# Kernel optimization log

Hardware: AMD Instinct MI355X
Metric: run time of the kernel (lower is better)

The kernel has to match this reference:

```python
import jax, jax.numpy as jnp
import numpy as np

B, T, C = 1, 1024, 2048
N = 64          # head_size
H = C // N      # 32 heads
D_W = 96        # max(32, round(1.8*sqrt(C)/32)*32)
D_A = 96
D_V = 64        # max(32, round(1.3*sqrt(C)/32)*32)
EPS = 1e-12     # F.normalize eps


def setup_inputs() -> dict:
    key = jax.random.key(0)
    ks = jax.random.split(key, 24)
    g = lambda i, shape, s=0.02: jax.random.normal(ks[i], shape, jnp.float32) * s
    return {
        "x": jax.random.normal(ks[0], (B, T, C), jnp.float32),
        "v_first": jax.random.normal(ks[1], (B, T, C), jnp.float32),
        "attention_mask": jnp.ones((B, T), jnp.float32),
        "w0": g(2, (1, 1, C), 0.1) - 0.5,
        "w1": g(3, (C, D_W)),
        "w2": g(4, (D_W, C)),
        "a0": g(5, (1, 1, C), 0.1),
        "a1": g(6, (C, D_A)),
        "a2": g(7, (D_A, C)),
        "v0": g(8, (1, 1, C), 0.1) + 1.0,
        "v1": g(9, (C, D_V)),
        "v2": g(10, (D_V, C)),
        "k_k": jnp.full((1, 1, C), 0.85, jnp.float32),
        "k_a": jnp.ones((1, 1, C), jnp.float32),
        "r_k": g(11, (H, N), 0.1),
        "Wr": g(12, (C, C)),   # pre-transposed Linear weights: y = x @ W
        "Wk": g(13, (C, C)),
        "Wv": g(14, (C, C)),
        "Wo": g(15, (C, C)),
    }


def rwkv7_scan(r, w, k, v, a, b, mask):
    """RWKV-7 recurrence (RUN_CUDA_RWKV7g). All of r,w,k,v,a,b are (B,T,C); mask (B,T).
    Per head: S_t = S_{t-1}*diag(exp(-exp(w_t))) + (S_{t-1} a_t) b_t^T + v_t k_t^T,
    out_t = S_t r_t.  Masked timesteps leave the state untouched."""
    rh, kh, vh, ah, bh = (t.reshape(B, T, H, N) for t in (r, k, v, a, b))
    dec = jnp.exp(-jnp.exp(w.reshape(B, T, H, N)))
    m = mask[:, :, None, None]
    dec = dec * m + (1.0 - m)            # no decay on padded steps
    kh, vh, ah, bh = kh * m, vh * m, ah * m, bh * m
    seq = tuple(jnp.moveaxis(t, 1, 0) for t in (dec, rh, kh, vh, ah, bh))
    s0 = jnp.zeros((B, H, N, N), r.dtype)  # state[...,i,j]: i=value dim, j=key dim

    def step(state, inp):
        d, rr, kk, vv, aa, bb = inp      # each (B,H,N)
        sa = jnp.einsum('bhij,bhj->bhi', state, aa)
        state = (state * d[:, :, None, :]
                 + sa[..., None] * bb[:, :, None, :]
                 + vv[..., None] * kk[:, :, None, :])
        return state, jnp.einsum('bhij,bhj->bhi', state, rr)

    _, out = jax.lax.scan(step, s0, seq)
    return jnp.moveaxis(out, 0, 1).reshape(B, T, C)


def reference(x, v_first, attention_mask, w0, w1, w2, a0, a1, a2,
              v0, v1, v2, k_k, k_a, r_k, Wr, Wk, Wv, Wo):
    r = x @ Wr
    k = x @ Wk
    v = x @ Wv
    w = -jax.nn.softplus(-(w0 + jnp.tanh(x @ w1) @ w2)) - 0.6
    # layer_id != 0: mix with v_first
    v = v + (v_first - v) * jax.nn.sigmoid(v0 + (x @ v1) @ v2)
    a = jax.nn.sigmoid(a0 + (x @ a1) @ a2)
    kk = k * k_k
    kkh = kk.reshape(B, T, H, N)
    kkh = kkh / jnp.maximum(jnp.linalg.norm(kkh, axis=-1, keepdims=True), EPS)
    kk = kkh.reshape(B, T, C)
    k = k * (1.0 + (a - 1.0) * k_a)
    o = rwkv7_scan(r, w, k, v, -kk, kk * a, attention_mask)
    rh, kh, vh = (t.reshape(B, T, H, N) for t in (r, k, v))
    o = o + ((rh * kh * r_k).sum(-1, keepdims=True) * vh).reshape(B, T, C)
    return (o @ Wo, v_first)
```

## Files before the change

### kernel.cpp

```cpp
#include <hip/hip_runtime.h>
#include <math.h>

#define T_LEN 1024
#define C_DIM 2048
#define H_N   32
#define HEAD  64
#define BTC   (T_LEN * C_DIM)
#define REC2  768
#define RKV_N 6144
#define NPAIR (T_LEN / 2)

typedef __attribute__((ext_vector_type(8))) __bf16 bf16x8;
typedef __attribute__((ext_vector_type(4))) float  f32x4;

__device__ __forceinline__ void gll16(const void* g, void* l) {
    __builtin_amdgcn_global_load_lds((const __attribute__((address_space(1))) void*)g,
                                     (__attribute__((address_space(3))) void*)l, 16, 0, 0);
}

__device__ __forceinline__ float hex_add(float x) {
    int a = __builtin_amdgcn_mov_dpp(__float_as_int(x), 0xB1, 0xF, 0xF, true);
    float y = x + __int_as_float(a);
    int b = __builtin_amdgcn_mov_dpp(__float_as_int(y), 0x4E, 0xF, 0xF, true);
    float z = y + __int_as_float(b);
    int c = __builtin_amdgcn_mov_dpp(__float_as_int(z), 0x141, 0xF, 0xF, true);
    float w = z + __int_as_float(c);
    int d = __builtin_amdgcn_mov_dpp(__float_as_int(w), 0x140, 0xF, 0xF, true);
    return w + __int_as_float(d);
}

__global__ void cast_bf16_k(const float* __restrict__ s, __bf16* __restrict__ d, int n) {
    int i = blockIdx.x * 256 + threadIdx.x;
    if (i < n) d[i] = (__bf16)s[i];
}
__global__ void tanh_cast_k(const float* __restrict__ s, __bf16* __restrict__ d, int n) {
    int i = blockIdx.x * 256 + threadIdx.x;
    if (i < n) d[i] = (__bf16)tanhf(s[i]);
}

__global__ void transpose_cast_k(const float* __restrict__ src, __bf16* __restrict__ dst,
                                 int R, int C) {
    __shared__ float tile[32][33];
    int c0 = blockIdx.x * 32, r0 = blockIdx.y * 32;
    int tx = threadIdx.x, ty = threadIdx.y;
#pragma unroll
    for (int i = 0; i < 32; i += 8)
        tile[ty + i][tx] = src[(size_t)(r0 + ty + i) * C + c0 + tx];
    __syncthreads();
#pragma unroll
    for (int i = 0; i < 32; i += 8)
        dst[(size_t)(c0 + ty + i) * R + r0 + tx] = (__bf16)tile[tx][ty + i];
}

__global__ __launch_bounds__(256) void gemm_lds_64x128(
    const __bf16* __restrict__ A, const __bf16* __restrict__ BT,
    float* __restrict__ O, int M, int N, int K) {
    __shared__ __bf16 As[64 * 32];
    __shared__ __bf16 Bs[128 * 32];
    int tid  = threadIdx.x;
    int lane = tid & 63;
    int wv   = tid >> 6;
    int m    = lane & 15;
    int q    = lane >> 4;
    int wr   = wv >> 1, wc = wv & 1;
    int row0 = blockIdx.x * 64;
    int col0 = blockIdx.y * 128;

    int srow  = tid >> 2;
    int skoff = (tid & 3) * 8;
    const __bf16* agp = A  + (size_t)(row0 + srow) * K + skoff;
    const __bf16* bgp = BT + (size_t)(col0 + srow) * K + skoff;
    __bf16* alp = As + (size_t)(tid & ~63) * 8;
    __bf16* blp = Bs + (size_t)(tid & ~63) * 8;

    f32x4 acc[2][4];
#pragma unroll
    for (int i = 0; i < 2; i++)
#pragma unroll
        for (int j = 0; j < 4; j++) acc[i][j] = {0.f, 0.f, 0.f, 0.f};

    for (int k0 = 0; k0 < K; k0 += 32) {
        gll16(agp + k0, alp);
        gll16(bgp + k0, blp);
        gll16(bgp + (size_t)64 * K + k0, blp + 64 * 32);
        __syncthreads();

        bf16x8 af[2], bfv[4];
#pragma unroll
        for (int i = 0; i < 2; i++)
            af[i] = *(const bf16x8*)&As[(wr * 32 + i * 16 + m) * 32 + q * 8];
#pragma unroll
        for (int j = 0; j < 4; j++)
            bfv[j] = *(const bf16x8*)&Bs[(wc * 64 + j * 16 + m) * 32 + q * 8];
#pragma unroll
        for (int i = 0; i < 2; i++)
#pragma unroll
            for (int j = 0; j < 4; j++)
                acc[i][j] = __builtin_amdgcn_mfma_f32_16x16x32_bf16(af[i], bfv[j], acc[i][j], 0, 0, 0);
        __syncthreads();
    }

#pragma unroll
    for (int i = 0; i < 2; i++) {
        int orow = row0 + wr * 32 + i * 16 + q * 4;
#pragma unroll
        for (int j = 0; j < 4; j++) {
            int ocol = col0 + wc * 64 + j * 16 + m;
#pragma unroll
            for (int t = 0; t < 4; t++)
                O[(size_t)(orow + t) * N + ocol] = acc[i][j][t];
        }
    }
}

__global__ __launch_bounds__(64) void gemm_bt_w16(
    const __bf16* __restrict__ A, const __bf16* __restrict__ BT,
    float* __restrict__ O, int M, int N, int K) {
    int lane = threadIdx.x & 63;
    int m = lane & 15, q = lane >> 4;
    int row0 = blockIdx.x * 16;
    int col0 = blockIdx.y * 16;
    const __bf16* ap = A  + (size_t)(row0 + m) * K + q * 8;
    const __bf16* bp = BT + (size_t)(col0 + m) * K + q * 8;
    f32x4 acc = {0.f,0.f,0.f,0.f};
    for (int k0 = 0; k0 < K; k0 += 32) {
        bf16x8 av = *(const bf16x8*)(ap + k0);
        bf16x8 bv = *(const bf16x8*)(bp + k0);
        acc = __builtin_amdgcn_mfma_f32_16x16x32_bf16(av, bv, acc, 0, 0, 0);
    }
    int orow = row0 + q * 4;
    int ocol = col0 + m;
#pragma unroll
    for (int i = 0; i < 4; i++)
        O[(size_t)(orow + i) * N + ocol] = acc[i];
}

__global__ __launch_bounds__(64) void prep2_k(
    float* __restrict__ rkv,
    const float* __restrict__ vfirst,
    const float* __restrict__ ywb, const float* __restrict__ yab,
    const float* __restrict__ yvb,
    float* __restrict__ pk,
    const float* __restrict__ w0, const float* __restrict__ a0,
    const float* __restrict__ v0, const float* __restrict__ k_k,
    const float* __restrict__ k_a, const float* __restrict__ amask) {
    int tp = blockIdx.x >> 5;
    int h  = blockIdx.x & 31;
    int n  = threadIdx.x;
    int cc = h * HEAD + n;

    float d[2], a[2], bv[2], k[2], v[2], r[2];
#pragma unroll
    for (int s = 0; s < 2; ++s) {
        int t = 2 * tp + s;
        int idx = t * C_DIM + cc;
        size_t idx6 = (size_t)t * RKV_N + cc;
        float m  = amask[t];
        float rr = rkv[idx6];
        float kv = rkv[idx6 + 2048];
        float vv = rkv[idx6 + 4096];
        float wv = w0[cc] + ywb[idx];
        float wfin = -log1pf(expf(-wv)) - 0.6f;
        float dec  = expf(-expf(wfin));
        float sv   = 1.f / (1.f + expf(-(v0[cc] + yvb[idx])));
        float vnew = fmaf(vfirst[idx] - vv, sv, vv);
        float av   = 1.f / (1.f + expf(-(a0[cc] + yab[idx])));
        float kkp  = kv * k_k[cc];
        float ss = kkp * kkp;
#pragma unroll
        for (int off = 32; off > 0; off >>= 1) ss += __shfl_xor(ss, off);
        float kkn  = kkp / fmaxf(sqrtf(ss), 1e-12f);
        float knew = kv * (1.f + (av - 1.f) * k_a[cc]);
        d[s]  = dec * m + (1.f - m);
        a[s]  = -kkn * m;
        bv[s] = kkn * av * m;
        k[s]  = knew * m;
        v[s]  = vnew * m;
        r[s]  = rr;
        rkv[idx6 + 2048] = knew;
        rkv[idx6 + 4096] = vnew;
    }

    float dba = bv[0] * a[1];
    float dka = k[0]  * a[1];
    float dbr = bv[0] * r[0];
    float dkr = k[0]  * r[0];
#pragma unroll
    for (int off = 32; off > 0; off >>= 1) {
        dba += __shfl_xor(dba, off);
        dka += __shfl_xor(dka, off);
        dbr += __shfl_xor(dbr, off);
        dkr += __shfl_xor(dkr, off);
    }

    size_t rec = ((size_t)tp * H_N + h) * REC2;
    pk[rec + n]        = a[0];
    pk[rec + 64 + n]   = d[0] * a[1];
    pk[rec + 128 + n]  = fmaf(dbr, a[0], d[0] * r[0]);
    pk[rec + 192 + n]  = d[0] * d[1];
    pk[rec + 256 + n]  = fmaf(dba, bv[1], d[1] * bv[0]);
    pk[rec + 320 + n]  = bv[1];
    pk[rec + 384 + n]  = fmaf(dka, bv[1], d[1] * k[0]);
    pk[rec + 448 + n]  = k[1];
    pk[rec + 512 + n]  = r[1];
    pk[rec + 576 + n]  = v[0];
    pk[rec + 640 + n]  = v[1];
    if (n == 0) pk[rec + 704] = dkr;
}

__global__ __launch_bounds__(64, 1) void scan_k(
    const float* __restrict__ pk, float* __restrict__ out) {
    int b = blockIdx.x;
    int xcd  = b & 7;
    int rest = b >> 3;
    int hi   = rest & 3;
    int g    = rest >> 2;
    int h    = xcd + 8 * hi;

    int lane = threadIdx.x;
    int r = lane >> 4;
    int c = lane & 15;
    int row = g * 4 + r;
    int jb  = c * 4;

    float S0 = 0.f, S1 = 0.f, S2 = 0.f, S3 = 0.f;

    float4 A1R[4], A2R[4], R1R[4], DDR[4], B1R[4], B2R[4], C1R[4], C2R[4], R2R[4];
    float  v1R[4], v2R[4], g1R[4];

    const size_t tstep = (size_t)H_N * REC2;
    const float* base = pk + (size_t)h * REC2;

#define LOADSLOT(S_, T_) do {                          \
    const float* L_ = base + (size_t)(T_) * tstep;     \
    A1R[S_] = *(const float4*)(L_ + jb);               \
    A2R[S_] = *(const float4*)(L_ + 64 + jb);          \
    R1R[S_] = *(const float4*)(L_ + 128 + jb);         \
    DDR[S_] = *(const float4*)(L_ + 192 + jb);         \
    B1R[S_] = *(const float4*)(L_ + 256 + jb);         \
    B2R[S_] = *(const float4*)(L_ + 320 + jb);         \
    C1R[S_] = *(const float4*)(L_ + 384 + jb);         \
    C2R[S_] = *(const float4*)(L_ + 448 + jb);         \
    R2R[S_] = *(const float4*)(L_ + 512 + jb);         \
    v1R[S_] = L_[576 + row];                           \
    v2R[S_] = L_[640 + row];                           \
    g1R[S_] = L_[704];                                 \
} while (0)

#pragma unroll
    for (int s = 0; s < 4; ++s) LOADSLOT(s, s);
    __builtin_amdgcn_sched_barrier(0);

    int off = h * HEAD;

#pragma unroll 1
    for (int tp0 = 0; tp0 < NPAIR; tp0 += 4) {
#pragma unroll
        for (int s = 0; s < 4; ++s) {
            int tp = tp0 + s;
            float4 A1v = A1R[s], A2v = A2R[s], R1v = R1R[s], DDv = DDR[s];
            float4 B1v = B1R[s], B2v = B2R[s], C1v = C1R[s], C2v = C2R[s];
            float4 R2v = R2R[s];
            float  vv1 = v1R[s], vv2 = v2R[s], gg1 = g1R[s];
            int tn = tp + 4;
            if (tn > NPAIR - 1) tn = NPAIR - 1;
            LOADSLOT(s, tn);
            __builtin_amdgcn_sched_barrier(0);

            float pa = fmaf(S0, A1v.x, S1 * A1v.y);
            float qa = fmaf(S2, A1v.z, S3 * A1v.w);
            float pb = fmaf(S0, A2v.x, S1 * A2v.y);
            float qb = fmaf(S2, A2v.z, S3 * A2v.w);
            float pr = fmaf(S0, R1v.x, S1 * R1v.y);
            float qr = fmaf(S2, R1v.z, S3 * R1v.w);
            float sa1 = hex_add(pa + qa);
            float sa2 = hex_add(pb + qb);
            float so1 = hex_add(pr + qr);
            if (c == 0) out[off + row] = fmaf(gg1, vv1, so1);

            float t0c = fmaf(vv1, C1v.x, vv2 * C2v.x);
            float t1c = fmaf(vv1, C1v.y, vv2 * C2v.y);
            float t2c = fmaf(vv1, C1v.z, vv2 * C2v.z);
            float t3c = fmaf(vv1, C1v.w, vv2 * C2v.w);
            float z0 = fmaf(sa1, B1v.x, t0c);
            float z1 = fmaf(sa1, B1v.y, t1c);
            float z2 = fmaf(sa1, B1v.z, t2c);
            float z3 = fmaf(sa1, B1v.w, t3c);
            float y0 = fmaf(sa2, B2v.x, z0);
            float y1 = fmaf(sa2, B2v.y, z1);
            float y2 = fmaf(sa2, B2v.z, z2);
            float y3 = fmaf(sa2, B2v.w, z3);
            S0 = fmaf(DDv.x, S0, y0);
            S1 = fmaf(DDv.y, S1, y1);
            S2 = fmaf(DDv.z, S2, y2);
            S3 = fmaf(DDv.w, S3, y3);

            float o0 = fmaf(S0, R2v.x, S1 * R2v.y);
            float o1 = fmaf(S2, R2v.z, S3 * R2v.w);
            float op = hex_add(o0 + o1);
            if (c == 0) out[off + C_DIM + row] = op;
            off += 2 * C_DIM;
            __builtin_amdgcn_sched_barrier(0);
        }
    }
#undef LOADSLOT
}

__global__ __launch_bounds__(64) void resid_k(
    const float* __restrict__ rkv, const float* __restrict__ souts,
    const float* __restrict__ r_k, const float* __restrict__ vfirst,
    __bf16* __restrict__ ob, float* __restrict__ dout) {
    int t = blockIdx.x >> 5;
    int h = blockIdx.x & 31;
    int n = threadIdx.x;
    int cc  = h * HEAD + n;
    int idx = t * C_DIM + cc;
    size_t idx6 = (size_t)t * RKV_N + cc;
    float s = rkv[idx6] * rkv[idx6 + 2048] * r_k[cc];
#pragma unroll
    for (int off = 32; off > 0; off >>= 1) s += __shfl_xor(s, off);
    float ov = souts[idx] + s * rkv[idx6 + 4096];
    ob[idx] = (__bf16)ov;
    dout[BTC + idx] = vfirst[idx];
}

extern "C" void kernel_launch(void* const* d_in, const int* in_sizes, int n_in,
                              void* d_out, int out_size, void* d_ws, size_t ws_size,
                              hipStream_t stream) {
    const float* x      = (const float*)d_in[0];
    const float* vfirst = (const float*)d_in[1];
    const float* amask  = (const float*)d_in[2];
    const float* w0 = (const float*)d_in[3];
    const float* w1 = (const float*)d_in[4];
    const float* w2 = (const float*)d_in[5];
    const float* a0 = (const float*)d_in[6];
    const float* a1 = (const float*)d_in[7];
    const float* a2 = (const float*)d_in[8];
    const float* v0 = (const float*)d_in[9];
    const float* v1 = (const float*)d_in[10];
    const float* v2 = (const float*)d_in[11];
    const float* k_k = (const float*)d_in[12];
    const float* k_a = (const float*)d_in[13];
    const float* r_k = (const float*)d_in[14];
    const float* Wr = (const float*)d_in[15];
    const float* Wk = (const float*)d_in[16];
    const float* Wv = (const float*)d_in[17];
    const float* Wo = (const float*)d_in[18];
    float* dout = (float*)d_out;

    char* wp = (char*)d_ws;
    auto alloc = [&](size_t bytes) -> void* {
        void* p = (void*)wp;
        wp += (bytes + 255) & ~(size_t)255;
        return p;
    };
    __bf16* xb   = (__bf16*)alloc((size_t)BTC * 2);
    __bf16* rkvT = (__bf16*)alloc((size_t)3 * C_DIM * C_DIM * 2);
    __bf16* WoT  = (__bf16*)alloc((size_t)C_DIM * C_DIM * 2);
    __bf16* w1T = (__bf16*)alloc((size_t)96 * C_DIM * 2);
    __bf16* a1T = (__bf16*)alloc((size_t)96 * C_DIM * 2);
    __bf16* v1T = (__bf16*)alloc((size_t)64 * C_DIM * 2);
    __bf16* w2T = (__bf16*)alloc((size_t)C_DIM * 96 * 2);
    __bf16* a2T = (__bf16*)alloc((size_t)C_DIM * 96 * 2);
    __bf16* v2T = (__bf16*)alloc((size_t)C_DIM * 64 * 2);
    float*  rkv = (float*)alloc((size_t)T_LEN * RKV_N * 4);
    float*  hw  = (float*)alloc((size_t)T_LEN * 96 * 4);
    float*  ha  = (float*)alloc((size_t)T_LEN * 96 * 4);
    float*  hv  = (float*)alloc((size_t)T_LEN * 64 * 4);
    __bf16* hwb = (__bf16*)alloc((size_t)T_LEN * 96 * 2);
    __bf16* hab = (__bf16*)alloc((size_t)T_LEN * 96 * 2);
    __bf16* hvb = (__bf16*)alloc((size_t)T_LEN * 64 * 2);
    float*  ywb = (float*)alloc((size_t)BTC * 4);
    float*  yab = (float*)alloc((size_t)BTC * 4);
    float*  yvb = (float*)alloc((size_t)BTC * 4);
    float*  pk  = (float*)alloc((size_t)NPAIR * H_N * REC2 * 4 + 4096);
    float*  souts = (float*)alloc((size_t)BTC * 4);
    __bf16* ob  = (__bf16*)alloc((size_t)BTC * 2);

    cast_bf16_k<<<dim3(BTC / 256), 256, 0, stream>>>(x, xb, BTC);

    dim3 tb(32, 8);
    transpose_cast_k<<<dim3(64, 64), tb, 0, stream>>>(Wr, rkvT, C_DIM, C_DIM);
    transpose_cast_k<<<dim3(64, 64), tb, 0, stream>>>(Wk, rkvT + (size_t)C_DIM * C_DIM, C_DIM, C_DIM);
    transpose_cast_k<<<dim3(64, 64), tb, 0, stream>>>(Wv, rkvT + (size_t)2 * C_DIM * C_DIM, C_DIM, C_DIM);
    transpose_cast_k<<<dim3(64, 64), tb, 0, stream>>>(Wo, WoT, C_DIM, C_DIM);
    transpose_cast_k<<<dim3(3, 64), tb, 0, stream>>>(w1, w1T, C_DIM, 96);
    transpose_cast_k<<<dim3(3, 64), tb, 0, stream>>>(a1, a1T, C_DIM, 96);
    transpose_cast_k<<<dim3(2, 64), tb, 0, stream>>>(v1, v1T, C_DIM, 64);
    transpose_cast_k<<<dim3(64, 3), tb, 0, stream>>>(w2, w2T, 96, C_DIM);
    transpose_cast_k<<<dim3(64, 3), tb, 0, stream>>>(a2, a2T, 96, C_DIM);
    transpose_cast_k<<<dim3(64, 2), tb, 0, stream>>>(v2, v2T, 64, C_DIM);

    gemm_lds_64x128<<<dim3(16, 48), 256, 0, stream>>>(xb, rkvT, rkv, T_LEN, RKV_N, C_DIM);

    gemm_bt_w16<<<dim3(64, 6), 64, 0, stream>>>(xb, w1T, hw, T_LEN, 96, C_DIM);
    gemm_bt_w16<<<dim3(64, 6), 64, 0, stream>>>(xb, a1T, ha, T_LEN, 96, C_DIM);
    gemm_bt_w16<<<dim3(64, 4), 64, 0, stream>>>(xb, v1T, hv, T_LEN, 64, C_DIM);

    tanh_cast_k<<<dim3((T_LEN * 96 + 255) / 256), 256, 0, stream>>>(hw, hwb, T_LEN * 96);
    cast_bf16_k<<<dim3((T_LEN * 96 + 255) / 256), 256, 0, stream>>>(ha, hab, T_LEN * 96);
    cast_bf16_k<<<dim3((T_LEN * 64 + 255) / 256), 256, 0, stream>>>(hv, hvb, T_LEN * 64);

    gemm_lds_64x128<<<dim3(16, 16), 256, 0, stream>>>(hwb, w2T, ywb, T_LEN, C_DIM, 96);
    gemm_lds_64x128<<<dim3(16, 16), 256, 0, stream>>>(hab, a2T, yab, T_LEN, C_DIM, 96);
    gemm_lds_64x128<<<dim3(16, 16), 256, 0, stream>>>(hvb, v2T, yvb, T_LEN, C_DIM, 64);

    prep2_k<<<dim3(NPAIR * H_N), 64, 0, stream>>>(rkv, vfirst, ywb, yab, yvb,
                                                  pk, w0, a0, v0, k_k, k_a, amask);

    scan_k<<<dim3(H_N * 16), 64, 0, stream>>>(pk, souts);

    resid_k<<<dim3(T_LEN * H_N), 64, 0, stream>>>(rkv, souts, r_k, vfirst, ob, dout);

    gemm_lds_64x128<<<dim3(16, 16), 256, 0, stream>>>(ob, WoT, dout, T_LEN, C_DIM, C_DIM);
}
```

Baseline: 528.1 us.

## Batch weight transposes and LoRA GEMMs into fewer launches, pack scan v/residual loads

Merges the ten transpose kernels into one z-indexed launch. The three first-stage LoRA GEMMs become one N=256 GEMM with a fused tanh/cast pass, and the three second-stage LoRA GEMMs become one z-batched launch. The scan record packs v1, v2 and the precomputed dkr*v into a single float4 per row, replacing three scalar loads and an fma. The aim is to cut launch count and scan load latency, at the cost of a larger pk record (REC2 768 to 832) and some early-exit blocks in the transpose grid.

New measurement: 475.4 us. 1.11x faster.

```diff
diff --git a/kernel.cpp b/kernel.cpp
--- a/kernel.cpp
+++ b/kernel.cpp
@@ -6,7 +6,7 @@
 #define H_N   32
 #define HEAD  64
 #define BTC   (T_LEN * C_DIM)
-#define REC2  768
+#define REC2  832
 #define RKV_N 6144
 #define NPAIR (T_LEN / 2)
 
@@ -33,15 +33,28 @@
     int i = blockIdx.x * 256 + threadIdx.x;
     if (i < n) d[i] = (__bf16)s[i];
 }
-__global__ void tanh_cast_k(const float* __restrict__ s, __bf16* __restrict__ d, int n) {
+
+__global__ void act_lora1_k(const float* __restrict__ s, __bf16* __restrict__ d) {
     int i = blockIdx.x * 256 + threadIdx.x;
-    if (i < n) d[i] = (__bf16)tanhf(s[i]);
-}
-
-__global__ void transpose_cast_k(const float* __restrict__ src, __bf16* __restrict__ dst,
-                                 int R, int C) {
+    float v = s[i];
+    if ((i & 255) < 96) v = tanhf(v);
+    d[i] = (__bf16)v;
+}
+
+struct TransBatch {
+    const float* s[10];
+    __bf16*      d[10];
+    int R[10];
+    int C[10];
+};
+__global__ void transpose_batch_k(TransBatch tb) {
+    int z = blockIdx.z;
+    const float* src = tb.s[z];
+    __bf16* dst = tb.d[z];
+    int R = tb.R[z], C = tb.C[z];
+    int c0 = blockIdx.x * 32, r0 = blockIdx.y * 32;
+    if (c0 >= C || r0 >= R) return;
     __shared__ float tile[32][33];
-    int c0 = blockIdx.x * 32, r0 = blockIdx.y * 32;
     int tx = threadIdx.x, ty = threadIdx.y;
 #pragma unroll
     for (int i = 0; i < 32; i += 8)
@@ -69,6 +82,78 @@
     int srow  = tid >> 2;
     int skoff = (tid & 3) * 8;
     const __bf16* agp = A  + (size_t)(row0 + srow) * K + skoff;
+    const __bf16* bgp = BT + (size_t)(col0 + srow) * K + skoff;
+    __bf16* alp = As + (size_t)(tid & ~63) * 8;
+    __bf16* blp = Bs + (size_t)(tid & ~63) * 8;
+
+    f32x4 acc[2][4];
+#pragma unroll
+    for (int i = 0; i < 2; i++)
+#pragma unroll
+        for (int j = 0; j < 4; j++) acc[i][j] = {0.f, 0.f, 0.f, 0.f};
+
+    for (int k0 = 0; k0 < K; k0 += 32) {
+        gll16(agp + k0, alp);
+        gll16(bgp + k0, blp);
+        gll16(bgp + (size_t)64 * K + k0, blp + 64 * 32);
+        __syncthreads();
+
+        bf16x8 af[2], bfv[4];
+#pragma unroll
+        for (int i = 0; i < 2; i++)
+            af[i] = *(const bf16x8*)&As[(wr * 32 + i * 16 + m) * 32 + q * 8];
+#pragma unroll
+        for (int j = 0; j < 4; j++)
+            bfv[j] = *(const bf16x8*)&Bs[(wc * 64 + j * 16 + m) * 32 + q * 8];
+#pragma unroll
+        for (int i = 0; i < 2; i++)
+#pragma unroll
+            for (int j = 0; j < 4; j++)
+                acc[i][j] = __builtin_amdgcn_mfma_f32_16x16x32_bf16(af[i], bfv[j], acc[i][j], 0, 0, 0);
+        __syncthreads();
+    }
+
+#pragma unroll
+    for (int i = 0; i < 2; i++) {
+        int orow = row0 + wr * 32 + i * 16 + q * 4;
+#pragma unroll
+        for (int j = 0; j < 4; j++) {
+            int ocol = col0 + wc * 64 + j * 16 + m;
+#pragma unroll
+            for (int t = 0; t < 4; t++)
+                O[(size_t)(orow + t) * N + ocol] = acc[i][j][t];
+        }
+    }
+}
+
+struct Lora2Cfg {
+    const __bf16* A[3];
+    const __bf16* BT[3];
+    float*        O[3];
+    int K[3];
+};
+__global__ __launch_bounds__(256) void gemm_lora2_k(Lora2Cfg cfg) {
+    const int LDA = 256, N = C_DIM;
+    int z = blockIdx.z;
+    const __bf16* A  = cfg.A[z];
+    const __bf16* BT = cfg.BT[z];
+    float* O = cfg.O[z];
+    int K = cfg.K[z];
+
+    __shared__ __bf16 As[64 * 32];
+    __shared__ __bf16 Bs[128 * 32];
+    int tid  = threadIdx.x;
+    int lane = tid & 63;
+    int wv   = tid >> 6;
+    int m    = lane & 15;
+    int q    = lane >> 4;
+    int wr   = wv >> 1, wc = wv & 1;
+    int row0 = blockIdx.x * 64;
+    int col0 = blockIdx.y * 128;
+
+    int srow  = tid >> 2;
+    int skoff = (tid & 3) * 8;
+    const __bf16* agp = A  + (size_t)(row0 + srow) * LDA + skoff;
     const __bf16* bgp = BT + (size_t)(col0 + srow) * K + skoff;
     __bf16* alp = As + (size_t)(tid & ~63) * 8;
     __bf16* blp = Bs + (size_t)(tid & ~63) * 8;
@@ -203,9 +288,8 @@
     pk[rec + 384 + n]  = fmaf(dka, bv[1], d[1] * k[0]);
     pk[rec + 448 + n]  = k[1];
     pk[rec + 512 + n]  = r[1];
-    pk[rec + 576 + n]  = v[0];
-    pk[rec + 640 + n]  = v[1];
-    if (n == 0) pk[rec + 704] = dkr;
+    float4 vr = {v[0], v[1], dkr * v[0], 0.f};
+    *(float4*)&pk[rec + 576 + n * 4] = vr;
 }
 
 __global__ __launch_bounds__(64, 1) void scan_k(
@@ -225,8 +309,7 @@
 
     float S0 = 0.f, S1 = 0.f, S2 = 0.f, S3 = 0.f;
 
-    float4 A1R[4], A2R[4], R1R[4], DDR[4], B1R[4], B2R[4], C1R[4], C2R[4], R2R[4];
-    float  v1R[4], v2R[4], g1R[4];
+    float4 A1R[4], A2R[4], R1R[4], DDR[4], B1R[4], B2R[4], C1R[4], C2R[4], R2R[4], VRR[4];
 
     const size_t tstep = (size_t)H_N * REC2;
     const float* base = pk + (size_t)h * REC2;
@@ -242,9 +325,7 @@
     C1R[S_] = *(const float4*)(L_ + 384 + jb);         \
     C2R[S_] = *(const float4*)(L_ + 448 + jb);         \
     R2R[S_] = *(const float4*)(L_ + 512 + jb);         \
-    v1R[S_] = L_[576 + row];                           \
-    v2R[S_] = L_[640 + row];                           \
-    g1R[S_] = L_[704];                                 \
+    VRR[S_] = *(const float4*)(L_ + 576 + row * 4);    \
 } while (0)
 
 #pragma unroll
@@ -260,13 +341,13 @@
             int tp = tp0 + s;
             float4 A1v = A1R[s], A2v = A2R[s], R1v = R1R[s], DDv = DDR[s];
             float4 B1v = B1R[s], B2v = B2R[s], C1v = C1R[s], C2v = C2R[s];
-            float4 R2v = R2R[s];
-            float  vv1 = v1R[s], vv2 = v2R[s], gg1 = g1R[s];
+            float4 R2v = R2R[s], vr = VRR[s];
             int tn = tp + 4;
             if (tn > NPAIR - 1) tn = NPAIR - 1;
             LOADSLOT(s, tn);
             __builtin_amdgcn_sched_barrier(0);
 
+            float vv1 = vr.x, vv2 = vr.y;
             float pa = fmaf(S0, A1v.x, S1 * A1v.y);
             float qa = fmaf(S2, A1v.z, S3 * A1v.w);
             float pb = fmaf(S0, A2v.x, S1 * A2v.y);
@@ -276,7 +357,7 @@
             float sa1 = hex_add(pa + qa);
             float sa2 = hex_add(pb + qb);
             float so1 = hex_add(pr + qr);
-            if (c == 0) out[off + row] = fmaf(gg1, vv1, so1);
+            if (c == 0) out[off + row] = so1 + vr.z;
 
             float t0c = fmaf(vv1, C1v.x, vv2 * C2v.x);
             float t1c = fmaf(vv1, C1v.y, vv2 * C2v.y);
@@ -354,22 +435,16 @@
         wp += (bytes + 255) & ~(size_t)255;
         return p;
     };
-    __bf16* xb   = (__bf16*)alloc((size_t)BTC * 2);
-    __bf16* rkvT = (__bf16*)alloc((size_t)3 * C_DIM * C_DIM * 2);
-    __bf16* WoT  = (__bf16*)alloc((size_t)C_DIM * C_DIM * 2);
-    __bf16* w1T = (__bf16*)alloc((size_t)96 * C_DIM * 2);
-    __bf16* a1T = (__bf16*)alloc((size_t)96 * C_DIM * 2);
-    __bf16* v1T = (__bf16*)alloc((size_t)64 * C_DIM * 2);
+    __bf16* xb     = (__bf16*)alloc((size_t)BTC * 2);
+    __bf16* rkvT   = (__bf16*)alloc((size_t)3 * C_DIM * C_DIM * 2);
+    __bf16* WoT    = (__bf16*)alloc((size_t)C_DIM * C_DIM * 2);
+    __bf16* lora1T = (__bf16*)alloc((size_t)256 * C_DIM * 2);
     __bf16* w2T = (__bf16*)alloc((size_t)C_DIM * 96 * 2);
     __bf16* a2T = (__bf16*)alloc((size_t)C_DIM * 96 * 2);
     __bf16* v2T = (__bf16*)alloc((size_t)C_DIM * 64 * 2);
     float*  rkv = (float*)alloc((size_t)T_LEN * RKV_N * 4);
-    float*  hw  = (float*)alloc((size_t)T_LEN * 96 * 4);
-    float*  ha  = (float*)alloc((size_t)T_LEN * 96 * 4);
-    float*  hv  = (float*)alloc((size_t)T_LEN * 64 * 4);
-    __bf16* hwb = (__bf16*)alloc((size_t)T_LEN * 96 * 2);
-    __bf16* hab = (__bf16*)alloc((size_t)T_LEN * 96 * 2);
-    __bf16* hvb = (__bf16*)alloc((size_t)T_LEN * 64 * 2);
+    float*  hall  = (float*)alloc((size_t)T_LEN * 256 * 4);
+    __bf16* hallb = (__bf16*)alloc((size_t)T_LEN * 256 * 2);
     float*  ywb = (float*)alloc((size_t)BTC * 4);
     float*  yab = (float*)alloc((size_t)BTC * 4);
     float*  yvb = (float*)alloc((size_t)BTC * 4);
@@ -379,31 +454,30 @@
 
     cast_bf16_k<<<dim3(BTC / 256), 256, 0, stream>>>(x, xb, BTC);
 
-    dim3 tb(32, 8);
-    transpose_cast_k<<<dim3(64, 64), tb, 0, stream>>>(Wr, rkvT, C_DIM, C_DIM);
-    transpose_cast_k<<<dim3(64, 64), tb, 0, stream>>>(Wk, rkvT + (size_t)C_DIM * C_DIM, C_DIM, C_DIM);
-    transpose_cast_k<<<dim3(64, 64), tb, 0, stream>>>(Wv, rkvT + (size_t)2 * C_DIM * C_DIM, C_DIM, C_DIM);
-    transpose_cast_k<<<dim3(64, 64), tb, 0, stream>>>(Wo, WoT, C_DIM, C_DIM);
-    transpose_cast_k<<<dim3(3, 64), tb, 0, stream>>>(w1, w1T, C_DIM, 96);
-    transpose_cast_k<<<dim3(3, 64), tb, 0, stream>>>(a1, a1T, C_DIM, 96);
-    transpose_cast_k<<<dim3(2, 64), tb, 0, stream>>>(v1, v1T, C_DIM, 64);
-    transpose_cast_k<<<dim3(64, 3), tb, 0, stream>>>(w2, w2T, 96, C_DIM);
-    transpose_cast_k<<<dim3(64, 3), tb, 0, stream>>>(a2, a2T, 96, C_DIM);
-    transpose_cast_k<<<dim3(64, 2), tb, 0, stream>>>(v2, v2T, 64, C_DIM);
+    TransBatch tb;
+    tb.s[0] = Wr; tb.d[0] = rkvT;                              tb.R[0] = C_DIM; tb.C[0] = C_DIM;
+    tb.s[1] = Wk; tb.d[1] = rkvT + (size_t)C_DIM * C_DIM;      tb.R[1] = C_DIM; tb.C[1] = C_DIM;
+    tb.s[2] = Wv; tb.d[2] = rkvT + (size_t)2 * C_DIM * C_DIM;  tb.R[2] = C_DIM; tb.C[2] = C_DIM;
+    tb.s[3] = Wo; tb.d[3] = WoT;                               tb.R[3] = C_DIM; tb.C[3] = C_DIM;
+    tb.s[4] = w1; tb.d[4] = lora1T;                            tb.R[4] = C_DIM; tb.C[4] = 96;
+    tb.s[5] = a1; tb.d[5] = lora1T + (size_t)96 * C_DIM;       tb.R[5] = C_DIM; tb.C[5] = 96;
+    tb.s[6] = v1; tb.d[6] = lora1T + (size_t)192 * C_DIM;      tb.R[6] = C_DIM; tb.C[6] = 64;
+    tb.s[7] = w2; tb.d[7] = w2T;                               tb.R[7] = 96;    tb.C[7] = C_DIM;
+    tb.s[8] = a2; tb.d[8] = a2T;                               tb.R[8] = 96;    tb.C[8] = C_DIM;
+    tb.s[9] = v2; tb.d[9] = v2T;                               tb.R[9] = 64;    tb.C[9] = C_DIM;
+    transpose_batch_k<<<dim3(64, 64, 10), dim3(32, 8), 0, stream>>>(tb);
 
     gemm_lds_64x128<<<dim3(16, 48), 256, 0, stream>>>(xb, rkvT, rkv, T_LEN, RKV_N, C_DIM);
 
-    gemm_bt_w16<<<dim3(64, 6), 64, 0, stream>>>(xb, w1T, hw, T_LEN, 96, C_DIM);
-    gemm_bt_w16<<<dim3(64, 6), 64, 0, stream>>>(xb, a1T, ha, T_LEN, 96, C_DIM);
-    gemm_bt_w16<<<dim3(64, 4), 64, 0, stream>>>(xb, v1T, hv, T_LEN, 64, C_DIM);
-
-    tanh_cast_k<<<dim3((T_LEN * 96 + 255) / 256), 256, 0, stream>>>(hw, hwb, T_LEN * 96);
-    cast_bf16_k<<<dim3((T_LEN * 96 + 255) / 256), 256, 0, stream>>>(ha, hab, T_LEN * 96);
-    cast_bf16_k<<<dim3((T_LEN * 64 + 255) / 256), 256, 0, stream>>>(hv, hvb, T_LEN * 64);
-
-    gemm_lds_64x128<<<dim3(16, 16), 256, 0, stream>>>(hwb, w2T, ywb, T_LEN, C_DIM, 96);
-    gemm_lds_64x128<<<dim3(16, 16), 256, 0, stream>>>(hab, a2T, yab, T_LEN, C_DIM, 96);
-    gemm_lds_64x128<<<dim3(16, 16), 256, 0, stream>>>(hvb, v2T, yvb, T_LEN, C_DIM, 64);
+    gemm_bt_w16<<<dim3(64, 16), 64, 0, stream>>>(xb, lora1T, hall, T_LEN, 256, C_DIM);
+
+    act_lora1_k<<<dim3(T_LEN * 256 / 256), 256, 0, stream>>>(hall, hallb);
+
+    Lora2Cfg lc;
+    lc.A[0] = hallb;       lc.BT[0] = w2T; lc.O[0] = ywb; lc.K[0] = 96;
+    lc.A[1] = hallb + 96;  lc.BT[1] = a2T; lc.O[1] = yab; lc.K[1] = 96;
+    lc.A[2] = hallb + 192; lc.BT[2] = v2T; lc.O[2] = yvb; lc.K[2] = 64;
+    gemm_lora2_k<<<dim3(16, 16, 3), 256, 0, stream>>>(lc);
 
     prep2_k<<<dim3(NPAIR * H_N), 64, 0, stream>>>(rkv, vfirst, ywb, yab, yvb,
                                                   pk, w0, a0, v0, k_k, k_a, amask);
```
